# Optimization experiments

Measured on AMD Instinct MI355X. Metric: run time of the kernel, lower is better.

Reference implementation:

```python
import jax, jax.numpy as jnp
import numpy as np

N_EMBD = 1024
NUM_EXPERTS = 8
TOP_K = 2
HIDDEN = 2048  # n_embd * hidden_mult(2)
AUX_COEF = 0.01
B, S = 4, 2048


def setup_inputs() -> dict:
    key = jax.random.key(0)
    k_x, k_g, k_w1, k_w2 = jax.random.split(key, 4)
    x = jax.random.normal(k_x, (B, S, N_EMBD), dtype=jnp.float32)
    # router gate: Linear(n_embd, num_experts, bias=False) -> weight (E, D), applied as x @ W^T
    gate_w = jax.random.uniform(k_g, (NUM_EXPERTS, N_EMBD), dtype=jnp.float32,
                                minval=-1.0 / np.sqrt(N_EMBD), maxval=1.0 / np.sqrt(N_EMBD))
    w1 = jax.random.uniform(k_w1, (NUM_EXPERTS, N_EMBD, HIDDEN), dtype=jnp.float32,
                            minval=-1.0 / np.sqrt(N_EMBD), maxval=1.0 / np.sqrt(N_EMBD))
    w2 = jax.random.uniform(k_w2, (NUM_EXPERTS, HIDDEN, N_EMBD), dtype=jnp.float32,
                            minval=-1.0 / np.sqrt(HIDDEN), maxval=1.0 / np.sqrt(HIDDEN))
    return {"x": x, "gate_w": gate_w, "w1": w1, "w2": w2}


def reference(x, gate_w, w1, w2):
    batch, seq, d = x.shape
    # router (token-level, no noise / eval path)
    router_logits = jnp.einsum('bsd,ed->bse', x, gate_w)          # (B,S,E)
    router_probs = jax.nn.softmax(router_logits, axis=-1)
    top_k_probs, top_k_indices = jax.lax.top_k(router_probs, TOP_K)  # (B,S,K)
    top_k_probs = top_k_probs / jnp.sum(top_k_probs, axis=-1, keepdims=True)

    # dense all-expert FFN (matches torch einsum pattern)
    x_flat = x.reshape(-1, d)                                      # (N,D), N=B*S
    hidden = jnp.einsum('nd,edh->neh', x_flat, w1)                 # (N,E,H)
    hidden = jax.nn.relu(hidden)
    expert_out = jnp.einsum('neh,ehd->ned', hidden, w2)            # (N,E,D)
    expert_out = expert_out.reshape(batch, seq, NUM_EXPERTS, d)    # (B,S,E,D)

    # gather selected experts and combine
    idx = top_k_indices[..., None]                                 # (B,S,K,1)
    selected = jnp.take_along_axis(expert_out, idx, axis=2)        # (B,S,K,D)
    output = jnp.sum(selected * top_k_probs[..., None], axis=2)    # (B,S,D)

    # load-balancing aux loss (Switch style)
    probs_flat = router_probs.reshape(-1, NUM_EXPERTS)             # (N,E)
    top_expert = jnp.argmax(probs_flat, axis=-1)                   # (N,)
    f = jnp.mean(jax.nn.one_hot(top_expert, NUM_EXPERTS, dtype=probs_flat.dtype), axis=0)
    P = jnp.mean(probs_flat, axis=0)
    aux_loss = AUX_COEF * NUM_EXPERTS * jnp.sum(f * P)
    return output, aux_loss
```

## Files before the change

kernel.cpp:

```cpp
#include <hip/hip_runtime.h>
#include <hip/hip_bf16.h>
#include <stdint.h>

#define N_TOK 8192
#define DIM   1024
#define HID   2048
#define NEXP  8
#define RB    256

typedef __bf16 bf16x8 __attribute__((ext_vector_type(8)));
typedef float  f32x4  __attribute__((ext_vector_type(4)));
typedef unsigned short u16x8 __attribute__((ext_vector_type(8)));
typedef unsigned short u16x4 __attribute__((ext_vector_type(4)));

__device__ __forceinline__ float bits2f(unsigned short u) {
    union { unsigned int i; float f; } c; c.i = ((unsigned int)u) << 16; return c.f;
}
__device__ __forceinline__ unsigned short f2bfbits(float f) {
    __hip_bfloat16 h = __float2bfloat16(f);
    return *(unsigned short*)&h;
}

__device__ __forceinline__ void load_lds16(const void* g, void* l) {
    __builtin_amdgcn_global_load_lds(
        (const __attribute__((address_space(1))) void*)g,
        (__attribute__((address_space(3))) void*)l,
        16, 0, 0);
}

__global__ __launch_bounds__(256) void fused_pre_k(
    const float* __restrict__ x,
    const float* __restrict__ gate,
    const float* __restrict__ w1,
    const float* __restrict__ w2,
    int* __restrict__ epack, float* __restrict__ pw,
    unsigned short* __restrict__ xb,
    int* __restrict__ H0, int* __restrict__ H1, float* __restrict__ Pblk,
    unsigned short* __restrict__ w1t, unsigned short* __restrict__ w2t)
{
    __shared__ __align__(16) union {
        struct { float gw[NEXP][16][64]; int h0[NEXP]; int h1[NEXP]; float p[NEXP]; } r;
        unsigned short tile[64][72];
    } S;
    const int tid = threadIdx.x;
    const int bx  = blockIdx.x;

    if (bx < RB) {
        if (tid < NEXP) { S.r.h0[tid] = 0; S.r.h1[tid] = 0; S.r.p[tid] = 0.f; }
        for (int idx = tid; idx < NEXP * DIM; idx += 256) {
            int e = idx >> 10, rem = idx & 1023, i = rem >> 6, l = rem & 63;
            S.r.gw[e][i][l] = gate[e * DIM + l * 16 + i];
        }
        __syncthreads();
        int w = tid >> 6, lane = tid & 63;
        float prAcc[NEXP];
        #pragma unroll
        for (int e = 0; e < NEXP; ++e) prAcc[e] = 0.f;
        for (int it = 0; it < 8; ++it) {
            int token = bx * 32 + w * 8 + it;
            const float* xr = x + (size_t)token * DIM + lane * 16;
            float xv[16];
            #pragma unroll
            for (int q = 0; q < 4; ++q) {
                float4 v = *(const float4*)(xr + q * 4);
                xv[q * 4 + 0] = v.x; xv[q * 4 + 1] = v.y; xv[q * 4 + 2] = v.z; xv[q * 4 + 3] = v.w;
            }
            {
                u16x8 o0, o1;
                #pragma unroll
                for (int i = 0; i < 8; ++i) { o0[i] = f2bfbits(xv[i]); o1[i] = f2bfbits(xv[8 + i]); }
                unsigned short* dst = xb + (size_t)token * DIM + lane * 16;
                *(u16x8*)dst = o0;
                *(u16x8*)(dst + 8) = o1;
            }
            float lg[NEXP];
            #pragma unroll
            for (int e = 0; e < NEXP; ++e) {
                float s = 0.f;
                #pragma unroll
                for (int i = 0; i < 16; ++i) s += xv[i] * S.r.gw[e][i][lane];
                lg[e] = s;
            }
            #pragma unroll
            for (int off = 32; off > 0; off >>= 1)
                #pragma unroll
                for (int e = 0; e < NEXP; ++e) lg[e] += __shfl_xor(lg[e], off);
            float mx = lg[0]; int am = 0;
            #pragma unroll
            for (int e = 1; e < NEXP; ++e) if (lg[e] > mx) { mx = lg[e]; am = e; }
            float pr[NEXP], se = 0.f;
            #pragma unroll
            for (int e = 0; e < NEXP; ++e) { pr[e] = __expf(lg[e] - mx); se += pr[e]; }
            float inv = 1.f / se;
            #pragma unroll
            for (int e = 0; e < NEXP; ++e) pr[e] *= inv;
            float m2 = -1.f; int a2 = 0;
            #pragma unroll
            for (int e = 0; e < NEXP; ++e) if (e != am && pr[e] > m2) { m2 = pr[e]; a2 = e; }
            float psum = pr[am] + m2;
            if (lane == 0) {
                epack[token] = am | (a2 << 4);
                pw[token * 2] = pr[am] / psum;
                pw[token * 2 + 1] = m2 / psum;
                atomicAdd(&S.r.h0[am], 1);
                atomicAdd(&S.r.h1[a2], 1);
                #pragma unroll
                for (int e = 0; e < NEXP; ++e) prAcc[e] += pr[e];
            }
        }
        if (lane == 0) {
            #pragma unroll
            for (int e = 0; e < NEXP; ++e) atomicAdd(&S.r.p[e], prAcc[e]);
        }
        __syncthreads();
        if (tid < NEXP) {
            H0[bx * NEXP + tid] = S.r.h0[tid];
            H1[bx * NEXP + tid] = S.r.h1[tid];
            Pblk[bx * NEXP + tid] = S.r.p[tid];
        }
        return;
    }

    int bT = bx - RB;
    const float* inp; unsigned short* outp;
    int R, C, r0, c0;
    if (bT < 4096) {
        int e = bT >> 9, rem = bT & 511;
        R = DIM; C = HID;
        inp = w1 + (size_t)e * R * C; outp = w1t + (size_t)e * R * C;
        r0 = (rem >> 5) << 6; c0 = (rem & 31) << 6;
    } else {
        int b2 = bT - 4096;
        int e = b2 >> 9, rem = b2 & 511;
        R = HID; C = DIM;
        inp = w2 + (size_t)e * R * C; outp = w2t + (size_t)e * R * C;
        r0 = (rem >> 4) << 6; c0 = (rem & 15) << 6;
    }
    {
        int r = tid >> 2, cseg = (tid & 3) * 16;
        const float* src = inp + (size_t)(r0 + r) * C + c0 + cseg;
        #pragma unroll
        for (int q = 0; q < 4; ++q) {
            float4 v = *(const float4*)(src + q * 4);
            S.tile[r][cseg + q * 4 + 0] = f2bfbits(v.x);
            S.tile[r][cseg + q * 4 + 1] = f2bfbits(v.y);
            S.tile[r][cseg + q * 4 + 2] = f2bfbits(v.z);
            S.tile[r][cseg + q * 4 + 3] = f2bfbits(v.w);
        }
    }
    __syncthreads();
    {
        int c = tid >> 2, rseg = (tid & 3) * 16;
        unsigned short* dst = outp + (size_t)(c0 + c) * R + r0 + rseg;
        #pragma unroll
        for (int h = 0; h < 2; ++h) {
            u16x8 o;
            #pragma unroll
            for (int i = 0; i < 8; ++i) o[i] = S.tile[rseg + h * 8 + i][c];
            *(u16x8*)(dst + h * 8) = o;
        }
    }
}

__global__ __launch_bounds__(256) void scan_k(
    const int* __restrict__ H0, const int* __restrict__ H1,
    const float* __restrict__ Pblk,
    int* __restrict__ bbL, int* __restrict__ counts, int* __restrict__ basep,
    float* __restrict__ aux)
{
    __shared__ int h0S[RB * NEXP], h1S[RB * NEXP], bbS[RB * NEXP];
    __shared__ float pSh[RB * NEXP];
    __shared__ int cS[NEXP], fS[NEXP];
    __shared__ float psS[NEXP];
    int tid = threadIdx.x;
    for (int i = tid; i < RB * NEXP; i += 256) { h0S[i] = H0[i]; h1S[i] = H1[i]; pSh[i] = Pblk[i]; }
    __syncthreads();
    if (tid < NEXP) {
        int run = 0, f = 0; float p = 0.f;
        for (int b = 0; b < RB; ++b) {
            int i = b * NEXP + tid;
            bbS[i] = run;
            run += h0S[i] + h1S[i];
            f += h0S[i];
            p += pSh[i];
        }
        cS[tid] = run; fS[tid] = f; psS[tid] = p;
        counts[tid] = run;
    }
    __syncthreads();
    if (tid == 0) {
        int b = 0; float s = 0.f;
        for (int e = 0; e < NEXP; ++e) {
            basep[e] = b; b += cS[e];
            s += (fS[e] * (1.f / 8192.f)) * (psS[e] * (1.f / 8192.f));
        }
        aux[0] = 0.01f * 8.f * s;
    }
    __syncthreads();
    for (int i = tid; i < RB * NEXP; i += 256) bbL[i] = bbS[i];
}

__global__ __launch_bounds__(256) void scatter_k(
    const int* __restrict__ epack, const int* __restrict__ bbL,
    int* __restrict__ tok_list, int* __restrict__ code)
{
    int tid = threadIdx.x;
    int w = tid >> 6, lane = tid & 63;
    int g = blockIdx.x * 4 + w;
    int token = g * 32 + (lane >> 1);
    int ep = epack[token];
    int e = (lane & 1) ? ((ep >> 4) & 0xF) : (ep & 0xF);
    unsigned long long lower = (lane == 0) ? 0ull : ((~0ull) >> (64 - lane));
    unsigned long long mymask = 0;
    #pragma unroll
    for (int ee = 0; ee < NEXP; ++ee) {
        unsigned long long m = __ballot(e == ee);
        if (ee == e) mymask = m;
    }
    int rank = __popcll(mymask & lower);
    int slot = bbL[g * NEXP + e] + rank;
    tok_list[e * N_TOK + slot] = token;
    code[token * 2 + (lane & 1)] = (e << 13) | slot;
}

#define VMW(Nv) asm volatile("s_waitcnt vmcnt(" #Nv ")" ::: "memory")
#define BARv()  asm volatile("s_barrier" ::: "memory")

template<bool GATHER, bool RELU, int KT>
__global__ __launch_bounds__(256, 2) void moe_gemm(
    const unsigned short* __restrict__ A,
    const unsigned short* __restrict__ B,
    unsigned short* __restrict__ O,
    const int* __restrict__ counts,
    const int* __restrict__ basep,
    const int* __restrict__ tok_list,
    const int N)
{
    constexpr int K = KT * 64;
    const int e = blockIdx.z;
    const int cnt = counts[e];
    const int m0 = blockIdx.y * 128;
    if (m0 >= cnt) return;
    const int n0 = blockIdx.x * 128;
    const int bas = basep[e];

    const int tid = threadIdx.x;
    const int w = tid >> 6, lane = tid & 63;
    const int wr = w >> 1, wc = w & 1;

    __shared__ __align__(16) unsigned short lds[32768];

    const int kc = ((tid & 3) ^ ((tid >> 3) & 3)) * 8;
    const int r0i = tid >> 2, r1i = 64 + (tid >> 2);
    const unsigned short *aRow0, *aRow1;
    if (GATHER) {
        int s0 = m0 + r0i, s1 = m0 + r1i;
        int t0 = (s0 < cnt) ? tok_list[e * N_TOK + s0] : 0;
        int t1 = (s1 < cnt) ? tok_list[e * N_TOK + s1] : 0;
        aRow0 = A + (size_t)t0 * K + kc;
        aRow1 = A + (size_t)t1 * K + kc;
    } else {
        int s0 = m0 + r0i; if (s0 > cnt - 1) s0 = cnt - 1;
        int s1 = m0 + r1i; if (s1 > cnt - 1) s1 = cnt - 1;
        aRow0 = A + (size_t)(bas + s0) * K + kc;
        aRow1 = A + (size_t)(bas + s1) * K + kc;
    }
    const unsigned short* Be = B + (size_t)e * N * K;
    const unsigned short* bRow0 = Be + (size_t)(n0 + r0i) * K + kc;
    const unsigned short* bRow1 = Be + (size_t)(n0 + r1i) * K + kc;

    f32x4 acc[4][4];
    #pragma unroll
    for (int i = 0; i < 4; ++i)
        #pragma unroll
        for (int j = 0; j < 4; ++j) acc[i][j] = f32x4{0.f, 0.f, 0.f, 0.f};

    const int quad = lane >> 4, ml = lane & 15;
    int offA[4], offB[4];
    #pragma unroll
    for (int i = 0; i < 4; ++i) {
        int Ra = wr * 64 + i * 16 + ml;
        offA[i] = Ra * 32 + ((quad ^ ((Ra >> 1) & 3)) * 8);
        int Rb = wc * 64 + i * 16 + ml;
        offB[i] = Rb * 32 + ((quad ^ ((Rb >> 1) & 3)) * 8);
    }

    auto stageG = [&](int tt, int h) {
        const int db = ((tt & 1) << 14) + (h << 12) + (tid << 3);
        const int toff = tt * 64 + h * 32;
        load_lds16(aRow0 + toff, &lds[db]);
        load_lds16(aRow1 + toff, &lds[db + 2048]);
        load_lds16(bRow0 + toff, &lds[db + 8192]);
        load_lds16(bRow1 + toff, &lds[db + 8192 + 2048]);
    };

    auto compute = [&](int bb, int ks) {
        const unsigned short* Lb = &lds[(bb << 14) + (ks << 12)];
        bf16x8 af[4], bfr[4];
        #pragma unroll
        for (int i = 0; i < 4; ++i) af[i] = *(const bf16x8*)&Lb[offA[i]];
        #pragma unroll
        for (int j = 0; j < 4; ++j) bfr[j] = *(const bf16x8*)&Lb[8192 + offB[j]];
        __builtin_amdgcn_s_setprio(1);
        #pragma unroll
        for (int i = 0; i < 4; ++i)
            #pragma unroll
            for (int j = 0; j < 4; ++j)
                acc[i][j] = __builtin_amdgcn_mfma_f32_16x16x32_bf16(af[i], bfr[j], acc[i][j], 0, 0, 0);
        __builtin_amdgcn_s_setprio(0);
        BARv();
    };

    stageG(0, 0); stageG(0, 1); stageG(1, 0);

    #pragma unroll 2
    for (int t = 0; t < KT - 2; ++t) {
        const int b = t & 1;
        stageG(t + 1, 1); VMW(12); BARv(); compute(b, 0);
        stageG(t + 2, 0); VMW(12); BARv(); compute(b, 1);
    }
    {
        const int bA = (KT - 2) & 1;
        stageG(KT - 1, 1); VMW(12); BARv(); compute(bA, 0);
        VMW(8);  BARv(); compute(bA, 1);
        const int bB = (KT - 1) & 1;
        VMW(4);  BARv(); compute(bB, 0);
        VMW(0);  BARv(); compute(bB, 1);
    }

    #pragma unroll
    for (int i = 0; i < 4; ++i) {
        int rbase = wr * 64 + i * 16 + quad * 4;
        #pragma unroll
        for (int r = 0; r < 4; ++r) {
            int slot = m0 + rbase + r;
            if (slot < cnt) {
                unsigned short* orow = O + (size_t)(bas + slot) * N + n0 + wc * 64 + ml;
                #pragma unroll
                for (int j = 0; j < 4; ++j) {
                    float v = acc[i][j][r];
                    if (RELU) v = v > 0.f ? v : 0.f;
                    orow[j * 16] = f2bfbits(v);
                }
            }
        }
    }
}

__global__ __launch_bounds__(256) void combine_k(
    const unsigned short* __restrict__ Y,
    const int* __restrict__ code, const float* __restrict__ pw,
    const int* __restrict__ basep,
    float* __restrict__ out)
{
    int t = blockIdx.x;
    int c0 = code[t * 2], c1 = code[t * 2 + 1];
    float p0 = pw[t * 2], p1 = pw[t * 2 + 1];
    size_t r0 = (size_t)(basep[c0 >> 13] + (c0 & 0x1FFF)) * DIM;
    size_t r1 = (size_t)(basep[c1 >> 13] + (c1 & 0x1FFF)) * DIM;
    int d = threadIdx.x * 4;
    u16x4 a = *(const u16x4*)(Y + r0 + d);
    u16x4 b = *(const u16x4*)(Y + r1 + d);
    float4 o;
    o.x = p0 * bits2f(a[0]) + p1 * bits2f(b[0]);
    o.y = p0 * bits2f(a[1]) + p1 * bits2f(b[1]);
    o.z = p0 * bits2f(a[2]) + p1 * bits2f(b[2]);
    o.w = p0 * bits2f(a[3]) + p1 * bits2f(b[3]);
    *(float4*)(out + (size_t)t * DIM + d) = o;
}

extern "C" void kernel_launch(void* const* d_in, const int* in_sizes, int n_in,
                              void* d_out, int out_size, void* d_ws, size_t ws_size,
                              hipStream_t stream)
{
    const float* x    = (const float*)d_in[0];
    const float* gate = (const float*)d_in[1];
    const float* w1   = (const float*)d_in[2];
    const float* w2   = (const float*)d_in[3];
    float* out = (float*)d_out;

    char* ws = (char*)d_ws;
    int*   counts   = (int*)(ws + 0);
    int*   basep    = (int*)(ws + 256);
    int*   epack    = (int*)(ws + 1024);
    int*   H0       = (int*)(ws + 1024 + 32768);
    int*   H1       = (int*)(ws + 1024 + 40960);
    float* Pblk     = (float*)(ws + 1024 + 49152);
    int*   bbL      = (int*)(ws + 1024 + 57344);
    int*   tok_list = (int*)(ws + 131072);
    int*   code     = (int*)(ws + 131072 + 262144);
    float* pw       = (float*)(ws + 131072 + 262144 + 65536);
    unsigned short* w1t    = (unsigned short*)(ws + (1 << 20));
    unsigned short* w2t    = (unsigned short*)(ws + (1 << 20) + 33554432);
    unsigned short* hidden = (unsigned short*)(ws + (1 << 20) + 67108864);
    unsigned short* xb     = (unsigned short*)(ws + (1 << 20) + 134217728);
    unsigned short* Y      = xb;

    fused_pre_k<<<RB + 8192, 256, 0, stream>>>(x, gate, w1, w2, epack, pw, xb,
                                               H0, H1, Pblk, w1t, w2t);
    scan_k<<<1, 256, 0, stream>>>(H0, H1, Pblk, bbL, counts, basep, out + (size_t)N_TOK * DIM);
    scatter_k<<<64, 256, 0, stream>>>(epack, bbL, tok_list, code);
    moe_gemm<true, true, DIM / 64><<<dim3(HID / 128, 64, NEXP), 256, 0, stream>>>(
        xb, w1t, hidden, counts, basep, tok_list, HID);
    moe_gemm<false, false, HID / 64><<<dim3(DIM / 128, 64, NEXP), 256, 0, stream>>>(
        hidden, w2t, Y, counts, basep, tok_list, DIM);
    combine_k<<<N_TOK, 256, 0, stream>>>(Y, code, pw, basep, out);
}
```

Before: 399.0 us.

## Enlarge MoE GEMM tiles to 256x256 with 512-thread blocks and 1D expert-interleaved grid

Replaces the 128x128 tile, 256-thread expert GEMM with a 256x256 tile, 8-wave kernel using 128KB of LDS double buffering and a full 64-wide K step per stage with an XOR swizzle. The grid becomes 1D with the expert index in the low bits so the experts' blocks interleave. Larger tiles raise arithmetic intensity and cut global and L2 traffic per FLOP. In exchange each wave holds more accumulator registers, occupancy per CU is lower, the pipeline is simpler with an extra barrier per K step, and tiles on uneven expert counts waste more work.

```diff
diff --git a/kernel.cpp b/kernel.cpp
--- a/kernel.cpp
+++ b/kernel.cpp
@@ -27,6 +27,11 @@
         (__attribute__((address_space(3))) void*)l,
         16, 0, 0);
 }
+
+#define VMW(Nv) asm volatile("s_waitcnt vmcnt(" #Nv ")" ::: "memory")
+#define BARv()  asm volatile("s_barrier" ::: "memory")
+#define LGKM0() do { asm volatile("s_waitcnt lgkmcnt(0)" ::: "memory"); \
+                     __builtin_amdgcn_sched_barrier(0); } while (0)
 
 __global__ __launch_bounds__(256) void fused_pre_k(
     const float* __restrict__ x,
@@ -223,11 +228,8 @@
     code[token * 2 + (lane & 1)] = (e << 13) | slot;
 }
 
-#define VMW(Nv) asm volatile("s_waitcnt vmcnt(" #Nv ")" ::: "memory")
-#define BARv()  asm volatile("s_barrier" ::: "memory")
-
-template<bool GATHER, bool RELU, int KT>
-__global__ __launch_bounds__(256, 2) void moe_gemm(
+template<bool GATHER, bool RELU, int KT, int NTL>
+__global__ __launch_bounds__(512, 2) void moe_gemm256(
     const unsigned short* __restrict__ A,
     const unsigned short* __restrict__ B,
     unsigned short* __restrict__ O,
@@ -237,110 +239,108 @@
     const int N)
 {
     constexpr int K = KT * 64;
-    const int e = blockIdx.z;
+    const int bid = blockIdx.x;
+    const int e  = bid & 7;
+    const int q  = bid >> 3;
+    const int m0 = (q >> NTL) * 256;
+    const int n0 = (q & ((1 << NTL) - 1)) * 256;
     const int cnt = counts[e];
-    const int m0 = blockIdx.y * 128;
     if (m0 >= cnt) return;
-    const int n0 = blockIdx.x * 128;
     const int bas = basep[e];
 
     const int tid = threadIdx.x;
-    const int w = tid >> 6, lane = tid & 63;
-    const int wr = w >> 1, wc = w & 1;
-
-    __shared__ __align__(16) unsigned short lds[32768];
-
-    const int kc = ((tid & 3) ^ ((tid >> 3) & 3)) * 8;
-    const int r0i = tid >> 2, r1i = 64 + (tid >> 2);
-    const unsigned short *aRow0, *aRow1;
-    if (GATHER) {
-        int s0 = m0 + r0i, s1 = m0 + r1i;
-        int t0 = (s0 < cnt) ? tok_list[e * N_TOK + s0] : 0;
-        int t1 = (s1 < cnt) ? tok_list[e * N_TOK + s1] : 0;
-        aRow0 = A + (size_t)t0 * K + kc;
-        aRow1 = A + (size_t)t1 * K + kc;
-    } else {
-        int s0 = m0 + r0i; if (s0 > cnt - 1) s0 = cnt - 1;
-        int s1 = m0 + r1i; if (s1 > cnt - 1) s1 = cnt - 1;
-        aRow0 = A + (size_t)(bas + s0) * K + kc;
-        aRow1 = A + (size_t)(bas + s1) * K + kc;
-    }
-    const unsigned short* Be = B + (size_t)e * N * K;
-    const unsigned short* bRow0 = Be + (size_t)(n0 + r0i) * K + kc;
-    const unsigned short* bRow1 = Be + (size_t)(n0 + r1i) * K + kc;
-
-    f32x4 acc[4][4];
-    #pragma unroll
-    for (int i = 0; i < 4; ++i)
+    const int wid = tid >> 6, lane = tid & 63;
+    const int wr = wid >> 2, wc = wid & 3;
+    const int q4 = lane >> 4, ml = lane & 15;
+
+    __shared__ __align__(16) unsigned short lds[65536];
+
+    const int u  = tid >> 3;
+    const int gk = (tid & 7) ^ (u & 7);
+    const unsigned short* aR[4];
+    #pragma unroll
+    for (int g = 0; g < 4; ++g) {
+        int slot = m0 + g * 64 + u;
+        int row;
+        if (GATHER) row = (slot < cnt) ? tok_list[e * N_TOK + slot] : 0;
+        else        row = bas + ((slot < cnt) ? slot : (cnt - 1));
+        aR[g] = A + (size_t)row * K + gk * 8;
+    }
+    const unsigned short* Be = B + (size_t)e * (size_t)N * K;
+    const unsigned short* bR = Be + (size_t)(n0 + u) * K + gk * 8;
+    const int std_ = tid * 8;
+
+    auto stage = [&](int b, int t) {
+        const int bo = b * 32768;
+        const int tk = t * 64;
+        #pragma unroll
+        for (int g = 0; g < 4; ++g)
+            load_lds16(aR[g] + tk, &lds[bo + g * 4096 + std_]);
+        #pragma unroll
+        for (int g = 0; g < 4; ++g)
+            load_lds16(bR + (size_t)g * 64 * K + tk, &lds[bo + 16384 + g * 4096 + std_]);
+    };
+
+    f32x4 acc[8][4];
+    #pragma unroll
+    for (int i = 0; i < 8; ++i)
         #pragma unroll
         for (int j = 0; j < 4; ++j) acc[i][j] = f32x4{0.f, 0.f, 0.f, 0.f};
 
-    const int quad = lane >> 4, ml = lane & 15;
-    int offA[4], offB[4];
-    #pragma unroll
-    for (int i = 0; i < 4; ++i) {
-        int Ra = wr * 64 + i * 16 + ml;
-        offA[i] = Ra * 32 + ((quad ^ ((Ra >> 1) & 3)) * 8);
-        int Rb = wc * 64 + i * 16 + ml;
-        offB[i] = Rb * 32 + ((quad ^ ((Rb >> 1) & 3)) * 8);
-    }
-
-    auto stageG = [&](int tt, int h) {
-        const int db = ((tt & 1) << 14) + (h << 12) + (tid << 3);
-        const int toff = tt * 64 + h * 32;
-        load_lds16(aRow0 + toff, &lds[db]);
-        load_lds16(aRow1 + toff, &lds[db + 2048]);
-        load_lds16(bRow0 + toff, &lds[db + 8192]);
-        load_lds16(bRow1 + toff, &lds[db + 8192 + 2048]);
+    const int cswz = ml & 7;
+    const int cp0 = (q4 ^ cswz) * 8;
+    const int cp1 = ((4 + q4) ^ cswz) * 8;
+    int offA[8], offB[4];
+    #pragma unroll
+    for (int ii = 0; ii < 8; ++ii) offA[ii] = (wr * 128 + ii * 16 + ml) * 64;
+    #pragma unroll
+    for (int jj = 0; jj < 4; ++jj) offB[jj] = 16384 + (wc * 64 + jj * 16 + ml) * 64;
+
+    auto compute = [&](int b) {
+        const int bo = b * 32768;
+        #pragma unroll
+        for (int kh = 0; kh < 2; ++kh) {
+            const int cp = kh ? cp1 : cp0;
+            bf16x8 bF[4];
+            #pragma unroll
+            for (int jj = 0; jj < 4; ++jj) bF[jj] = *(const bf16x8*)&lds[bo + offB[jj] + cp];
+            #pragma unroll
+            for (int ii = 0; ii < 8; ++ii) {
+                bf16x8 aF = *(const bf16x8*)&lds[bo + offA[ii] + cp];
+                __builtin_amdgcn_s_setprio(1);
+                #pragma unroll
+                for (int jj = 0; jj < 4; ++jj)
+                    acc[ii][jj] = __builtin_amdgcn_mfma_f32_16x16x32_bf16(
+                        aF, bF[jj], acc[ii][jj], 0, 0, 0);
+                __builtin_amdgcn_s_setprio(0);
+            }
+        }
     };
 
-    auto compute = [&](int bb, int ks) {
-        const unsigned short* Lb = &lds[(bb << 14) + (ks << 12)];
-        bf16x8 af[4], bfr[4];
-        #pragma unroll
-        for (int i = 0; i < 4; ++i) af[i] = *(const bf16x8*)&Lb[offA[i]];
-        #pragma unroll
-        for (int j = 0; j < 4; ++j) bfr[j] = *(const bf16x8*)&Lb[8192 + offB[j]];
-        __builtin_amdgcn_s_setprio(1);
-        #pragma unroll
-        for (int i = 0; i < 4; ++i)
-            #pragma unroll
-            for (int j = 0; j < 4; ++j)
-                acc[i][j] = __builtin_amdgcn_mfma_f32_16x16x32_bf16(af[i], bfr[j], acc[i][j], 0, 0, 0);
-        __builtin_amdgcn_s_setprio(0);
+    stage(0, 0);
+    for (int t = 0; t < KT; ++t) {
+        const int b = t & 1;
+        if (t + 1 < KT) { stage(b ^ 1, t + 1); VMW(8); }
+        else            { VMW(0); }
         BARv();
-    };
-
-    stageG(0, 0); stageG(0, 1); stageG(1, 0);
-
-    #pragma unroll 2
-    for (int t = 0; t < KT - 2; ++t) {
-        const int b = t & 1;
-        stageG(t + 1, 1); VMW(12); BARv(); compute(b, 0);
-        stageG(t + 2, 0); VMW(12); BARv(); compute(b, 1);
-    }
-    {
-        const int bA = (KT - 2) & 1;
-        stageG(KT - 1, 1); VMW(12); BARv(); compute(bA, 0);
-        VMW(8);  BARv(); compute(bA, 1);
-        const int bB = (KT - 1) & 1;
-        VMW(4);  BARv(); compute(bB, 0);
-        VMW(0);  BARv(); compute(bB, 1);
-    }
-
-    #pragma unroll
-    for (int i = 0; i < 4; ++i) {
-        int rbase = wr * 64 + i * 16 + quad * 4;
+        compute(b);
+        LGKM0();
+        BARv();
+    }
+
+    #pragma unroll
+    for (int ii = 0; ii < 8; ++ii) {
+        int rbase = wr * 128 + ii * 16 + q4 * 4;
         #pragma unroll
         for (int r = 0; r < 4; ++r) {
             int slot = m0 + rbase + r;
             if (slot < cnt) {
                 unsigned short* orow = O + (size_t)(bas + slot) * N + n0 + wc * 64 + ml;
                 #pragma unroll
-                for (int j = 0; j < 4; ++j) {
-                    float v = acc[i][j][r];
+                for (int jj = 0; jj < 4; ++jj) {
+                    float v = acc[ii][jj][r];
                     if (RELU) v = v > 0.f ? v : 0.f;
-                    orow[j * 16] = f2bfbits(v);
+                    orow[jj * 16] = f2bfbits(v);
                 }
             }
         }
@@ -400,9 +400,9 @@
                                                H0, H1, Pblk, w1t, w2t);
     scan_k<<<1, 256, 0, stream>>>(H0, H1, Pblk, bbL, counts, basep, out + (size_t)N_TOK * DIM);
     scatter_k<<<64, 256, 0, stream>>>(epack, bbL, tok_list, code);
-    moe_gemm<true, true, DIM / 64><<<dim3(HID / 128, 64, NEXP), 256, 0, stream>>>(
+    moe_gemm256<true, true, DIM / 64, 3><<<NEXP * 32 * 8, 512, 0, stream>>>(
         xb, w1t, hidden, counts, basep, tok_list, HID);
-    moe_gemm<false, false, HID / 64><<<dim3(DIM / 128, 64, NEXP), 256, 0, stream>>>(
+    moe_gemm256<false, false, HID / 64, 2><<<NEXP * 32 * 4, 512, 0, stream>>>(
         hidden, w2t, Y, counts, basep, tok_list, DIM);
     combine_k<<<N_TOK, 256, 0, stream>>>(Y, code, pw, basep, out);
 }
```

After: 425.0 us. 6.5% more time.
